# Kernel optimization log

Hardware: AMD Instinct MI355X
Metric: run time of the kernel (lower is better)

## Reference

```python
import jax, jax.numpy as jnp
import numpy as np

T = 5          # temporal_window_size
B = 512        # batch (graphs per timestep)
NA = 16        # num_agents (nodes per graph)
S = 64         # num_belief_states
A = 16         # action_dim
HID = 64       # hidden_dim per head
H = 4          # num_attn_heads
FD = HID * H   # 256, feature_dim
LAT = 128      # latent_dim
N = B * NA     # total nodes per timestep
FIN = S + A    # node feature dim
NEG_SLOPE = 0.2


def _edge_index():
    i, j = np.meshgrid(np.arange(NA), np.arange(NA), indexing='ij')
    m = i != j
    src_l, dst_l = i[m], j[m]                      # 240 intra-clique edges
    off = (np.arange(B) * NA)[:, None]
    src = (src_l[None] + off).ravel()
    dst = (dst_l[None] + off).ravel()
    loops = np.arange(N)                           # PyG GATConv add_self_loops=True
    src = np.concatenate([src, loops])
    dst = np.concatenate([dst, loops])
    return jnp.asarray(np.stack([src, dst]), dtype=jnp.int64)


def setup_inputs() -> dict:
    key = jax.random.key(0)
    ks = jax.random.split(key, 24)
    xav = lambda k, shp: jax.random.normal(k, shp, jnp.float32) * np.float32(np.sqrt(2.0 / (shp[0] + shp[-1])))
    return {
        'signals': jax.random.normal(ks[0], (T, B, S), jnp.float32),
        'neighbor_actions': jax.random.normal(ks[1], (T, B, NA * A), jnp.float32),
        'lin_w0': xav(ks[2], (FD, FIN)),
        'att_src0': xav(ks[3], (H, HID)),
        'att_dst0': xav(ks[4], (H, HID)),
        'bias0': jnp.zeros((FD,), jnp.float32),
        'lin_w1': xav(ks[5], (FD, FD)),
        'att_src1': xav(ks[6], (H, HID)),
        'att_dst1': xav(ks[7], (H, HID)),
        'bias1': jnp.zeros((FD,), jnp.float32),
        'in_proj_w': xav(ks[8], (3 * FD, FD)),
        'in_proj_b': jnp.zeros((3 * FD,), jnp.float32),
        'out_proj_w': xav(ks[9], (FD, FD)),
        'out_proj_b': jnp.zeros((FD,), jnp.float32),
        'w_mean': xav(ks[10], (LAT, FD)),
        'b_mean': jnp.zeros((LAT,), jnp.float32),
        'w_logvar': xav(ks[11], (LAT, FD)),
        'b_logvar': jnp.zeros((LAT,), jnp.float32),
        'w_belief': xav(ks[12], (S, FD)),
        'b_belief': jnp.zeros((S,), jnp.float32),
        'edge_index': _edge_index(),
    }


def _segment_softmax(e, seg, num_segments):
    # e: [E, T, H]; softmax over edges sharing the same target node.
    m = jax.ops.segment_max(e, seg, num_segments=num_segments)
    e = jnp.exp(e - m[seg])
    s = jax.ops.segment_sum(e, seg, num_segments=num_segments)
    return e / s[seg]


def _gat(x, src, dst, w, a_src, a_dst, b):
    # x: [N, T, Fin] -> [N, T, H*HID]   (PyG GATConv, concat heads)
    xl = jnp.einsum('ntf,of->nto', x, w).reshape(N, T, H, HID)
    e_src = jnp.einsum('nthc,hc->nth', xl, a_src)[src]   # [E, T, H]
    e_dst = jnp.einsum('nthc,hc->nth', xl, a_dst)[dst]
    e = jax.nn.leaky_relu(e_src + e_dst, NEG_SLOPE)
    alpha = _segment_softmax(e, dst, N)                  # per-target softmax
    out = jax.ops.segment_sum(alpha[..., None] * xl[src], dst, num_segments=N)
    return out.reshape(N, T, FD) + b


def reference(signals, neighbor_actions, lin_w0, att_src0, att_dst0, bias0,
              lin_w1, att_src1, att_dst1, bias1, in_proj_w, in_proj_b,
              out_proj_w, out_proj_b, w_mean, b_mean, w_logvar, b_logvar,
              w_belief, b_belief, edge_index):
    # --- _construct_graph (vectorized over time window + batch) ---
    acts = neighbor_actions.reshape(T, B, NA, A)
    beliefs = jnp.zeros((T, B, NA, S), signals.dtype).at[:, :, 0, :].set(signals)
    nodes = jnp.concatenate([beliefs, acts], -1).reshape(T, N, FIN)
    nodes = jnp.transpose(nodes, (1, 0, 2))              # [N, T, FIN]
    src, dst = edge_index[0], edge_index[1]
    x = jax.nn.relu(_gat(nodes, src, dst, lin_w0, att_src0, att_dst0, bias0))
    x = jax.nn.relu(_gat(x, src, dst, lin_w1, att_src1, att_dst1, bias1))
    # --- ego-node sequence: nodes 0, NA, 2*NA, ... ---
    seq = x[::NA]                                        # [B, T, FD]
    # --- temporal MultiheadAttention (batch_first, eval) ---
    qkv = seq @ in_proj_w.T + in_proj_b
    q, k, v = jnp.split(qkv, 3, axis=-1)
    dh = FD // H
    q = q.reshape(B, T, H, dh); k = k.reshape(B, T, H, dh); v = v.reshape(B, T, H, dh)
    scores = jnp.einsum('bqhd,bkhd->bhqk', q, k) / jnp.sqrt(jnp.asarray(dh, seq.dtype))
    # torch float attn_mask is ADDITIVE: mask[i,j]=1 if j<=i else 0
    mask = (jnp.arange(T)[:, None] >= jnp.arange(T)[None, :]).astype(seq.dtype)
    attn = jax.nn.softmax(scores + mask[None, None], axis=-1)
    ctx = jnp.einsum('bhqk,bkhd->bqhd', attn, v).reshape(B, T, FD)
    ctx = ctx @ out_proj_w.T + out_proj_b
    feat = ctx[:, -1]                                    # [B, FD]
    # --- heads ---
    mean = feat @ w_mean.T + b_mean
    logvar = feat @ w_logvar.T + b_logvar
    belief = jax.nn.softmax(feat @ w_belief.T + b_belief, axis=-1)
    return (mean, logvar, belief)
```

## Files before the change

### kernel.cpp

```cpp
#include <hip/hip_runtime.h>
#include <hip/hip_bf16.h>


__device__ __forceinline__ float wave_sum64(float v) {
    #pragma unroll
    for (int off = 32; off > 0; off >>= 1) v += __shfl_xor(v, off, 64);
    return v;
}
__device__ __forceinline__ float wave_max64(float v) {
    #pragma unroll
    for (int off = 32; off > 0; off >>= 1) v = fmaxf(v, __shfl_xor(v, off, 64));
    return v;
}

__global__ __launch_bounds__(256) void k_pre(
    const float* __restrict__ w0, const float* __restrict__ w1,
    const float* __restrict__ wip, const float* __restrict__ wop,
    const float* __restrict__ wm, const float* __restrict__ wlv,
    const float* __restrict__ wb,
    const float* __restrict__ as0, const float* __restrict__ ad0,
    const float* __restrict__ as1, const float* __restrict__ ad1,
    float* __restrict__ tws,
    float* __restrict__ u1, float* __restrict__ ud1,
    float* __restrict__ pa0, float* __restrict__ pd0)
{
    const int tid = threadIdx.x;
    if (blockIdx.x < 1680) {
        int i = blockIdx.x * 256 + tid;
        float v;
        if (i < 16384) {
            int k = i >> 8, n = i & 255;
            v = w0[n * 80 + k];
        } else if (i < 20480) {
            int j = i - 16384; int k = j >> 8, n = j & 255;
            v = w0[n * 80 + 64 + k];
        } else if (i < 86016) {
            int j = i - 20480; int k = j >> 8, n = j & 255;
            v = w1[n * 256 + k];
        } else if (i < 282624) {
            int j = i - 86016; int k = j / 768, n = j - k * 768;
            v = wip[n * 256 + k];
        } else if (i < 348160) {
            int j = i - 282624; int k = j >> 8, n = j & 255;
            v = wop[n * 256 + k];
        } else {
            int j = i - 348160; int k = j / 320, o = j - k * 320;
            if (o < 128)      v = wm[o * 256 + k];
            else if (o < 256) v = wlv[(o - 128) * 256 + k];
            else              v = wb[(o - 256) * 256 + k];
        }
        tws[i] = v;
        return;
    }
    for (int q = 0; q < 4; q++) {
        int idx = q * 256 + tid;
        int h = idx >> 8, k = idx & 255;
        float su = 0.f, sd = 0.f;
        for (int c = 0; c < 64; c++) {
            float wv = w1[(h * 64 + c) * 256 + k];
            su = fmaf(as1[h * 64 + c], wv, su);
            sd = fmaf(ad1[h * 64 + c], wv, sd);
        }
        u1[idx] = su; ud1[idx] = sd;
    }
    if (tid < 64) {
        int h = tid >> 4, k = tid & 15;
        float su = 0.f, sd = 0.f;
        for (int c = 0; c < 64; c++) {
            float wv = w0[(h * 64 + c) * 80 + 64 + k];
            su = fmaf(as0[h * 64 + c], wv, su);
            sd = fmaf(ad0[h * 64 + c], wv, sd);
        }
        pa0[tid] = su; pd0[tid] = sd;
    }
}

__global__ __launch_bounds__(256) void k_gat(
    const float* __restrict__ sig,
    const float* __restrict__ nact,
    const float* __restrict__ W0sT,
    const float* __restrict__ W0aT,
    const float* __restrict__ W1T,
    const float* __restrict__ u1g, const float* __restrict__ ud1g,
    const float* __restrict__ pa0g, const float* __restrict__ pd0g,
    const float* __restrict__ as0, const float* __restrict__ ad0,
    const float* __restrict__ b0, const float* __restrict__ b1,
    float* __restrict__ seqf)
{
    __shared__ __align__(16) char smem[37168];
    float* actL    = (float*)(smem + 0);
    float* sigL    = (float*)(smem + 1024);
    float* u1L     = (float*)(smem + 1280);
    float* ud1L    = (float*)(smem + 5440);
    float* pa0L    = (float*)(smem + 9600);
    float* pd0L    = (float*)(smem + 9856);
    float* sSL     = (float*)(smem + 10112);
    float* dSL     = (float*)(smem + 10128);
    float* es0L    = (float*)(smem + 10144);
    float* ed0L    = (float*)(smem + 10400);
    float* espL    = (float*)(smem + 10656);
    float* es1L    = (float*)(smem + 11680);
    float* edpL    = (float*)(smem + 11936);
    float* edL     = (float*)(smem + 12000);
    float* alpha1L = (float*)(smem + 12016);
    float* a0L     = (float*)(smem + 12272);
    float* zL      = (float*)(smem + 16368);
    float* x1L     = (float*)(smem + 20528);

    const int tid = threadIdx.x;
    const int bg = blockIdx.x;
    const int b = bg / 5, g = bg - b * 5;
    const int n = tid, w = tid >> 6, lane = tid & 63;

    if (tid < 64) sigL[tid] = sig[(g * 512 + b) * 64 + tid];
    actL[tid] = nact[(g * 512 + b) * 256 + tid];
    #pragma unroll
    for (int q = 0; q < 4; q++) {
        int idx = q * 256 + tid;
        int h = idx >> 8, k = idx & 255;
        u1L[h * 260 + k] = u1g[idx];
        ud1L[h * 260 + k] = ud1g[idx];
    }
    if (tid >= 64 && tid < 128) {
        pa0L[tid - 64] = pa0g[tid - 64];
        pd0L[tid - 64] = pd0g[tid - 64];
    }
    __syncthreads();

    float S = 0.f;
    {
        const float4* sig4 = (const float4*)sigL;
        #pragma unroll 4
        for (int i = 0; i < 16; i++) {
            float4 sv = sig4[i];
            S = fmaf(sv.x, W0sT[(i * 4 + 0) * 256 + n], S);
            S = fmaf(sv.y, W0sT[(i * 4 + 1) * 256 + n], S);
            S = fmaf(sv.z, W0sT[(i * 4 + 2) * 256 + n], S);
            S = fmaf(sv.w, W0sT[(i * 4 + 3) * 256 + n], S);
        }
        float ps = wave_sum64(S * as0[n]);
        float pd_ = wave_sum64(S * ad0[n]);
        if (lane == 0) { sSL[w] = ps; dSL[w] = pd_; }
    }
    __syncthreads();

    if (tid < 64) {
        int m = tid >> 2, h = tid & 3;
        float su = (m == 0) ? sSL[h] : 0.f;
        float sd = (m == 0) ? dSL[h] : 0.f;
        #pragma unroll
        for (int k = 0; k < 16; k++) {
            float av = actL[m * 16 + k];
            su = fmaf(av, pa0L[h * 16 + k], su);
            sd = fmaf(av, pd0L[h * 16 + k], sd);
        }
        es0L[m * 4 + h] = su; ed0L[m * 4 + h] = sd;
    }
    __syncthreads();

    if (tid < 64) {
        int h = tid >> 4, j = tid & 15;
        float ej = ed0L[j * 4 + h];
        float e[16], m = -1e30f;
        #pragma unroll
        for (int s = 0; s < 16; s++) {
            float x = es0L[s * 4 + h] + ej;
            x = (x >= 0.f) ? x : 0.2f * x;
            e[s] = x; m = fmaxf(m, x);
        }
        float sum = 0.f;
        #pragma unroll
        for (int s = 0; s < 16; s++) { e[s] = __expf(e[s] - m); sum += e[s]; }
        float inv = 1.f / sum;
        float4* a04 = (float4*)(a0L + h * 256 + j * 16);
        #pragma unroll
        for (int s4 = 0; s4 < 4; s4++)
            a04[s4] = make_float4(e[s4 * 4] * inv, e[s4 * 4 + 1] * inv,
                                  e[s4 * 4 + 2] * inv, e[s4 * 4 + 3] * inv);
    }
    __syncthreads();

    float x1r[16];
    {
        const int h = w;
        float wr[16];
        #pragma unroll
        for (int k = 0; k < 16; k++) wr[k] = W0aT[k * 256 + n];
        const float4* act4 = (const float4*)actL;
        float xl0r[16];
        #pragma unroll
        for (int s = 0; s < 16; s++) {
            float a = 0.f;
            #pragma unroll
            for (int q = 0; q < 4; q++) {
                float4 av = act4[s * 4 + q];
                a = fmaf(av.x, wr[q * 4 + 0], a);
                a = fmaf(av.y, wr[q * 4 + 1], a);
                a = fmaf(av.z, wr[q * 4 + 2], a);
                a = fmaf(av.w, wr[q * 4 + 3], a);
            }
            xl0r[s] = a;
        }
        xl0r[0] += S;
        const float b0v = b0[n];
        const float4* a04 = (const float4*)(a0L + h * 256);
        #pragma unroll
        for (int j = 0; j < 16; j++) {
            float acc = b0v;
            #pragma unroll
            for (int s4 = 0; s4 < 4; s4++) {
                float4 a4 = a04[j * 4 + s4];
                acc = fmaf(a4.x, xl0r[s4 * 4 + 0], acc);
                acc = fmaf(a4.y, xl0r[s4 * 4 + 1], acc);
                acc = fmaf(a4.z, xl0r[s4 * 4 + 2], acc);
                acc = fmaf(a4.w, xl0r[s4 * 4 + 3], acc);
            }
            x1r[j] = fmaxf(acc, 0.f);
            x1L[j * 260 + n] = x1r[j];
        }
    }
    __syncthreads();

    {
        const int m = tid & 15, h = (tid >> 4) & 3, p = tid >> 6;
        const float4* x4p = (const float4*)(x1L + m * 260 + p * 64);
        const float4* u4p = (const float4*)(u1L + h * 260 + p * 64);
        float a = 0.f;
        #pragma unroll
        for (int i = 0; i < 16; i++) {
            float4 xv = x4p[i], uv = u4p[i];
            a = fmaf(xv.x, uv.x, a);
            a = fmaf(xv.y, uv.y, a);
            a = fmaf(xv.z, uv.z, a);
            a = fmaf(xv.w, uv.w, a);
        }
        espL[m * 16 + h * 4 + p] = a;
        if (m == 0) {
            const float4* ud4p = (const float4*)(ud1L + h * 260 + p * 64);
            float ad = 0.f;
            #pragma unroll
            for (int i = 0; i < 16; i++) {
                float4 xv = x4p[i], uv = ud4p[i];
                ad = fmaf(xv.x, uv.x, ad);
                ad = fmaf(xv.y, uv.y, ad);
                ad = fmaf(xv.z, uv.z, ad);
                ad = fmaf(xv.w, uv.w, ad);
            }
            edpL[h * 4 + p] = ad;
        }
    }
    __syncthreads();
    if (tid < 64) {
        int m = tid >> 2, h = tid & 3;
        const float* e = espL + m * 16 + h * 4;
        es1L[m * 4 + h] = e[0] + e[1] + e[2] + e[3];
    }
    if (tid < 4)
        edL[tid] = edpL[tid * 4] + edpL[tid * 4 + 1] + edpL[tid * 4 + 2] + edpL[tid * 4 + 3];
    __syncthreads();

    if (tid < 4) {
        int h = tid;
        float ej = edL[h];
        float e[16], m = -1e30f;
        #pragma unroll
        for (int s = 0; s < 16; s++) {
            float x = es1L[s * 4 + h] + ej;
            x = (x >= 0.f) ? x : 0.2f * x;
            e[s] = x; m = fmaxf(m, x);
        }
        float sum = 0.f;
        #pragma unroll
        for (int s = 0; s < 16; s++) { e[s] = __expf(e[s] - m); sum += e[s]; }
        float inv = 1.f / sum;
        #pragma unroll
        for (int s = 0; s < 16; s++) alpha1L[h * 16 + s] = e[s] * inv;
    }
    __syncthreads();

    {
        const float4* a14 = (const float4*)alpha1L;
        #pragma unroll
        for (int hh = 0; hh < 4; hh++) {
            float zv = 0.f;
            #pragma unroll
            for (int s4 = 0; s4 < 4; s4++) {
                float4 a4 = a14[hh * 4 + s4];
                zv = fmaf(a4.x, x1r[s4 * 4 + 0], zv);
                zv = fmaf(a4.y, x1r[s4 * 4 + 1], zv);
                zv = fmaf(a4.z, x1r[s4 * 4 + 2], zv);
                zv = fmaf(a4.w, x1r[s4 * 4 + 3], zv);
            }
            zL[hh * 260 + n] = zv;
        }
    }
    __syncthreads();

    {
        const float4* zh = (const float4*)(zL + w * 260);
        float acc = b1[n];
        #pragma unroll 8
        for (int i = 0; i < 64; i++) {
            float4 z4 = zh[i];
            acc = fmaf(z4.x, W1T[(i * 4 + 0) * 256 + n], acc);
            acc = fmaf(z4.y, W1T[(i * 4 + 1) * 256 + n], acc);
            acc = fmaf(z4.z, W1T[(i * 4 + 2) * 256 + n], acc);
            acc = fmaf(z4.w, W1T[(i * 4 + 3) * 256 + n], acc);
        }
        seqf[bg * 256 + n] = fmaxf(acc, 0.f);
    }
}

__global__ __launch_bounds__(768) void k_stage2(
    const float* __restrict__ seqf,
    const float* __restrict__ wipT,
    const float* __restrict__ bip,
    const float* __restrict__ wopT,
    const float* __restrict__ bop,
    const float* __restrict__ whT,
    const float* __restrict__ bm, const float* __restrict__ blv,
    const float* __restrict__ bb,
    float* __restrict__ out)
{
    __shared__ float sseq[2][5][256];
    __shared__ float kL[2][5][256], vL[2][5][256], qL[2][256];
    __shared__ float ctxL[2][256], featL[2][256];
    __shared__ float beliefL[2][64];
    const int tid = threadIdx.x;
    const int b0 = blockIdx.x * 2;

    {
        float* sflat = &sseq[0][0][0];
        for (int i = tid; i < 2560; i += 768)
            sflat[i] = seqf[b0 * 1280 + i];
    }
    __syncthreads();

    {
        const int kind = tid >> 8, n = tid & 255;
        if (kind == 0) {
            float a0 = 0.f, a1 = 0.f;
            for (int k = 0; k < 256; k++) {
                float wv = wipT[k * 768 + n];
                a0 = fmaf(sseq[0][4][k], wv, a0);
                a1 = fmaf(sseq[1][4][k], wv, a1);
            }
            float bv = bip[n];
            qL[0][n] = a0 + bv; qL[1][n] = a1 + bv;
        } else {
            const float* wcol = wipT + kind * 256 + n;
            float acc[2][5];
            #pragma unroll
            for (int gb = 0; gb < 2; gb++)
                #pragma unroll
                for (int t = 0; t < 5; t++) acc[gb][t] = 0.f;
            for (int k = 0; k < 256; k++) {
                float wv = wcol[k * 768];
                #pragma unroll
                for (int gb = 0; gb < 2; gb++) {
                    #pragma unroll
                    for (int t = 0; t < 5; t++)
                        acc[gb][t] = fmaf(sseq[gb][t][k], wv, acc[gb][t]);
                }
            }
            float bv = bip[kind * 256 + n];
            float* dst = (kind == 1) ? &kL[0][0][0] : &vL[0][0][0];
            #pragma unroll
            for (int gb = 0; gb < 2; gb++)
                #pragma unroll
                for (int t = 0; t < 5; t++)
                    dst[gb * 1280 + t * 256 + n] = acc[gb][t] + bv;
        }
    }
    __syncthreads();

    if (tid < 512) {
        const int gb = tid >> 8, col = tid & 255;
        float q4 = qL[gb][col];
        float sc[5];
        #pragma unroll
        for (int t = 0; t < 5; t++)
            sc[t] = wave_sum64(q4 * kL[gb][t][col]) * 0.125f;
        float m = sc[0];
        #pragma unroll
        for (int t = 1; t < 5; t++) m = fmaxf(m, sc[t]);
        float p[5], sum = 0.f;
        #pragma unroll
        for (int t = 0; t < 5; t++) { p[t] = __expf(sc[t] - m); sum += p[t]; }
        float inv = 1.f / sum, cv = 0.f;
        #pragma unroll
        for (int t = 0; t < 5; t++) cv = fmaf(p[t], vL[gb][t][col], cv);
        ctxL[gb][col] = cv * inv;
    }
    __syncthreads();

    if (tid < 512) {
        const int gb = tid >> 8, n = tid & 255;
        float acc = 0.f;
        for (int k = 0; k < 256; k++)
            acc = fmaf(ctxL[gb][k], wopT[k * 256 + n], acc);
        featL[gb][n] = acc + bop[n];
    }
    __syncthreads();

    if (tid < 640) {
        const int gb = tid / 320, j = tid - gb * 320;
        float acc = 0.f;
        for (int k = 0; k < 256; k++)
            acc = fmaf(featL[gb][k], whT[k * 320 + j], acc);
        if (j < 128) {
            out[(b0 + gb) * 128 + j] = acc + bm[j];
        } else if (j < 256) {
            out[65536 + (b0 + gb) * 128 + (j - 128)] = acc + blv[j - 128];
        } else {
            beliefL[gb][j - 256] = acc + bb[j - 256];
        }
    }
    __syncthreads();

    if (tid < 128) {
        int gb = tid >> 6, lane = tid & 63;
        float lg = beliefL[gb][lane];
        float m = wave_max64(lg);
        float e = __expf(lg - m);
        float s = wave_sum64(e);
        out[131072 + (b0 + gb) * 64 + lane] = e / s;
    }
}

extern "C" void kernel_launch(void* const* d_in, const int* in_sizes, int n_in,
                              void* d_out, int out_size, void* d_ws, size_t ws_size,
                              hipStream_t stream) {
    const float* sig  = (const float*)d_in[0];
    const float* nact = (const float*)d_in[1];
    const float* w0   = (const float*)d_in[2];
    const float* as0  = (const float*)d_in[3];
    const float* ad0  = (const float*)d_in[4];
    const float* b0   = (const float*)d_in[5];
    const float* w1   = (const float*)d_in[6];
    const float* as1  = (const float*)d_in[7];
    const float* ad1  = (const float*)d_in[8];
    const float* b1   = (const float*)d_in[9];
    const float* wip  = (const float*)d_in[10];
    const float* bip  = (const float*)d_in[11];
    const float* wop  = (const float*)d_in[12];
    const float* bop  = (const float*)d_in[13];
    const float* wm   = (const float*)d_in[14];
    const float* bm   = (const float*)d_in[15];
    const float* wlv  = (const float*)d_in[16];
    const float* blv  = (const float*)d_in[17];
    const float* wb   = (const float*)d_in[18];
    const float* bb   = (const float*)d_in[19];

    float* ws    = (float*)d_ws;
    float* seqf  = ws;
    float* tws   = ws + 655360;
    float* W0sT  = tws;
    float* W0aT  = tws + 16384;
    float* W1T   = tws + 20480;
    float* wipT  = tws + 86016;
    float* wopT  = tws + 282624;
    float* whT   = tws + 348160;
    float* u1    = ws + 1085440;
    float* ud1   = ws + 1086464;
    float* pa0   = ws + 1087488;
    float* pd0   = ws + 1087552;

    k_pre   <<<1681, 256, 0, stream>>>(w0, w1, wip, wop, wm, wlv, wb,
                                       as0, ad0, as1, ad1,
                                       tws, u1, ud1, pa0, pd0);
    k_gat   <<<2560, 256, 0, stream>>>(sig, nact, W0sT, W0aT, W1T,
                                       u1, ud1, pa0, pd0, as0, ad0, b0, b1, seqf);
    k_stage2<<<256, 768, 0, stream>>>(seqf, wipT, bip, wopT, bop, whT,
                                      bm, blv, bb, (float*)d_out);
}
```

Before: 201.2 us.

## Make GAT layer-0 attention per-wave and batch weight loads in k_gat

Layer-0 attention logits and softmax are now computed inside each wave for its own head, using the wave-wide reductions directly. This removes three block-wide barriers and the sS/dS staging buffers. The layer-1 softmax is folded into wave 0, which drops one more barrier. Global weight loads for W0s and W1 are grouped 16 at a time to expose more memory-level parallelism, and launch bounds request 4 blocks per CU, which may constrain register allocation.

```diff
diff --git a/kernel.cpp b/kernel.cpp
--- a/kernel.cpp
+++ b/kernel.cpp
@@ -75,7 +75,7 @@
     }
 }
 
-__global__ __launch_bounds__(256) void k_gat(
+__global__ __launch_bounds__(256, 4) void k_gat(
     const float* __restrict__ sig,
     const float* __restrict__ nact,
     const float* __restrict__ W0sT,
@@ -87,25 +87,22 @@
     const float* __restrict__ b0, const float* __restrict__ b1,
     float* __restrict__ seqf)
 {
-    __shared__ __align__(16) char smem[37168];
+    __shared__ __align__(16) char smem[37120];
     float* actL    = (float*)(smem + 0);
     float* sigL    = (float*)(smem + 1024);
     float* u1L     = (float*)(smem + 1280);
     float* ud1L    = (float*)(smem + 5440);
     float* pa0L    = (float*)(smem + 9600);
     float* pd0L    = (float*)(smem + 9856);
-    float* sSL     = (float*)(smem + 10112);
-    float* dSL     = (float*)(smem + 10128);
-    float* es0L    = (float*)(smem + 10144);
-    float* ed0L    = (float*)(smem + 10400);
-    float* espL    = (float*)(smem + 10656);
-    float* es1L    = (float*)(smem + 11680);
-    float* edpL    = (float*)(smem + 11936);
-    float* edL     = (float*)(smem + 12000);
-    float* alpha1L = (float*)(smem + 12016);
-    float* a0L     = (float*)(smem + 12272);
-    float* zL      = (float*)(smem + 16368);
-    float* x1L     = (float*)(smem + 20528);
+    float* es0w    = (float*)(smem + 10112);
+    float* ed0w    = (float*)(smem + 10368);
+    float* espL    = (float*)(smem + 10624);
+    float* es1L    = (float*)(smem + 11648);
+    float* edpL    = (float*)(smem + 11904);
+    float* alpha1L = (float*)(smem + 11968);
+    float* a0L     = (float*)(smem + 12224);
+    float* zL      = (float*)(smem + 16320);
+    float* x1L     = (float*)(smem + 20480);
 
     const int tid = threadIdx.x;
     const int bg = blockIdx.x;
@@ -130,59 +127,70 @@
     float S = 0.f;
     {
         const float4* sig4 = (const float4*)sigL;
-        #pragma unroll 4
-        for (int i = 0; i < 16; i++) {
-            float4 sv = sig4[i];
-            S = fmaf(sv.x, W0sT[(i * 4 + 0) * 256 + n], S);
-            S = fmaf(sv.y, W0sT[(i * 4 + 1) * 256 + n], S);
-            S = fmaf(sv.z, W0sT[(i * 4 + 2) * 256 + n], S);
-            S = fmaf(sv.w, W0sT[(i * 4 + 3) * 256 + n], S);
-        }
-        float ps = wave_sum64(S * as0[n]);
-        float pd_ = wave_sum64(S * ad0[n]);
-        if (lane == 0) { sSL[w] = ps; dSL[w] = pd_; }
-    }
-    __syncthreads();
-
-    if (tid < 64) {
-        int m = tid >> 2, h = tid & 3;
-        float su = (m == 0) ? sSL[h] : 0.f;
-        float sd = (m == 0) ? dSL[h] : 0.f;
-        #pragma unroll
-        for (int k = 0; k < 16; k++) {
-            float av = actL[m * 16 + k];
-            su = fmaf(av, pa0L[h * 16 + k], su);
-            sd = fmaf(av, pd0L[h * 16 + k], sd);
-        }
-        es0L[m * 4 + h] = su; ed0L[m * 4 + h] = sd;
-    }
-    __syncthreads();
-
-    if (tid < 64) {
-        int h = tid >> 4, j = tid & 15;
-        float ej = ed0L[j * 4 + h];
+        #pragma unroll
+        for (int i = 0; i < 4; i++) {
+            float wv[16];
+            #pragma unroll
+            for (int j = 0; j < 16; j++)
+                wv[j] = W0sT[(i * 16 + j) * 256 + n];
+            #pragma unroll
+            for (int q = 0; q < 4; q++) {
+                float4 sv = sig4[i * 4 + q];
+                S = fmaf(wv[q * 4 + 0], sv.x, S);
+                S = fmaf(wv[q * 4 + 1], sv.y, S);
+                S = fmaf(wv[q * 4 + 2], sv.z, S);
+                S = fmaf(wv[q * 4 + 3], sv.w, S);
+            }
+        }
+    }
+    const float sS = wave_sum64(S * as0[n]);
+    const float dS = wave_sum64(S * ad0[n]);
+
+    if (lane < 16) {
+        const int m = lane;
+        float su = (m == 0) ? sS : 0.f;
+        float sd = (m == 0) ? dS : 0.f;
+        const float4* act4 = (const float4*)(actL + m * 16);
+        const float4* pa4  = (const float4*)(pa0L + w * 16);
+        const float4* pd4  = (const float4*)(pd0L + w * 16);
+        #pragma unroll
+        for (int q = 0; q < 4; q++) {
+            float4 av = act4[q], pv = pa4[q], dv = pd4[q];
+            su = fmaf(av.x, pv.x, su); su = fmaf(av.y, pv.y, su);
+            su = fmaf(av.z, pv.z, su); su = fmaf(av.w, pv.w, su);
+            sd = fmaf(av.x, dv.x, sd); sd = fmaf(av.y, dv.y, sd);
+            sd = fmaf(av.z, dv.z, sd); sd = fmaf(av.w, dv.w, sd);
+        }
+        es0w[w * 16 + m] = su;
+        ed0w[w * 16 + m] = sd;
+    }
+    if (lane < 16) {
+        const int j = lane;
+        float ej = ed0w[w * 16 + j];
         float e[16], m = -1e30f;
-        #pragma unroll
-        for (int s = 0; s < 16; s++) {
-            float x = es0L[s * 4 + h] + ej;
-            x = (x >= 0.f) ? x : 0.2f * x;
-            e[s] = x; m = fmaxf(m, x);
+        const float4* es4 = (const float4*)(es0w + w * 16);
+        #pragma unroll
+        for (int s4 = 0; s4 < 4; s4++) {
+            float4 ev = es4[s4];
+            float x;
+            x = ev.x + ej; x = (x >= 0.f) ? x : 0.2f * x; e[s4*4+0] = x; m = fmaxf(m, x);
+            x = ev.y + ej; x = (x >= 0.f) ? x : 0.2f * x; e[s4*4+1] = x; m = fmaxf(m, x);
+            x = ev.z + ej; x = (x >= 0.f) ? x : 0.2f * x; e[s4*4+2] = x; m = fmaxf(m, x);
+            x = ev.w + ej; x = (x >= 0.f) ? x : 0.2f * x; e[s4*4+3] = x; m = fmaxf(m, x);
         }
         float sum = 0.f;
         #pragma unroll
         for (int s = 0; s < 16; s++) { e[s] = __expf(e[s] - m); sum += e[s]; }
         float inv = 1.f / sum;
-        float4* a04 = (float4*)(a0L + h * 256 + j * 16);
+        float4* a04 = (float4*)(a0L + w * 256 + j * 16);
         #pragma unroll
         for (int s4 = 0; s4 < 4; s4++)
             a04[s4] = make_float4(e[s4 * 4] * inv, e[s4 * 4 + 1] * inv,
                                   e[s4 * 4 + 2] * inv, e[s4 * 4 + 3] * inv);
     }
-    __syncthreads();
 
     float x1r[16];
     {
-        const int h = w;
         float wr[16];
         #pragma unroll
         for (int k = 0; k < 16; k++) wr[k] = W0aT[k * 256 + n];
@@ -203,7 +211,7 @@
         }
         xl0r[0] += S;
         const float b0v = b0[n];
-        const float4* a04 = (const float4*)(a0L + h * 256);
+        const float4* a04 = (const float4*)(a0L + w * 256);
         #pragma unroll
         for (int j = 0; j < 16; j++) {
             float acc = b0v;
@@ -250,31 +258,30 @@
         }
     }
     __syncthreads();
-    if (tid < 64) {
-        int m = tid >> 2, h = tid & 3;
-        const float* e = espL + m * 16 + h * 4;
-        es1L[m * 4 + h] = e[0] + e[1] + e[2] + e[3];
-    }
-    if (tid < 4)
-        edL[tid] = edpL[tid * 4] + edpL[tid * 4 + 1] + edpL[tid * 4 + 2] + edpL[tid * 4 + 3];
-    __syncthreads();
-
-    if (tid < 4) {
-        int h = tid;
-        float ej = edL[h];
-        float e[16], m = -1e30f;
-        #pragma unroll
-        for (int s = 0; s < 16; s++) {
-            float x = es1L[s * 4 + h] + ej;
-            x = (x >= 0.f) ? x : 0.2f * x;
-            e[s] = x; m = fmaxf(m, x);
-        }
-        float sum = 0.f;
-        #pragma unroll
-        for (int s = 0; s < 16; s++) { e[s] = __expf(e[s] - m); sum += e[s]; }
-        float inv = 1.f / sum;
-        #pragma unroll
-        for (int s = 0; s < 16; s++) alpha1L[h * 16 + s] = e[s] * inv;
+
+    if (w == 0) {
+        {
+            const int m = lane >> 2, h = lane & 3;
+            const float* e = espL + m * 16 + h * 4;
+            es1L[m * 4 + h] = e[0] + e[1] + e[2] + e[3];
+        }
+        if (lane < 4) {
+            const int h = lane;
+            float ej = edpL[h * 4] + edpL[h * 4 + 1] + edpL[h * 4 + 2] + edpL[h * 4 + 3];
+            float e[16], m = -1e30f;
+            #pragma unroll
+            for (int s = 0; s < 16; s++) {
+                float x = es1L[s * 4 + h] + ej;
+                x = (x >= 0.f) ? x : 0.2f * x;
+                e[s] = x; m = fmaxf(m, x);
+            }
+            float sum = 0.f;
+            #pragma unroll
+            for (int s = 0; s < 16; s++) { e[s] = __expf(e[s] - m); sum += e[s]; }
+            float inv = 1.f / sum;
+            #pragma unroll
+            for (int s = 0; s < 16; s++) alpha1L[h * 16 + s] = e[s] * inv;
+        }
     }
     __syncthreads();
 
@@ -299,13 +306,19 @@
     {
         const float4* zh = (const float4*)(zL + w * 260);
         float acc = b1[n];
-        #pragma unroll 8
-        for (int i = 0; i < 64; i++) {
-            float4 z4 = zh[i];
-            acc = fmaf(z4.x, W1T[(i * 4 + 0) * 256 + n], acc);
-            acc = fmaf(z4.y, W1T[(i * 4 + 1) * 256 + n], acc);
-            acc = fmaf(z4.z, W1T[(i * 4 + 2) * 256 + n], acc);
-            acc = fmaf(z4.w, W1T[(i * 4 + 3) * 256 + n], acc);
+        for (int i = 0; i < 16; i++) {
+            float wv[16];
+            #pragma unroll
+            for (int j = 0; j < 16; j++)
+                wv[j] = W1T[(i * 16 + j) * 256 + n];
+            #pragma unroll
+            for (int q = 0; q < 4; q++) {
+                float4 z4 = zh[i * 4 + q];
+                acc = fmaf(wv[q * 4 + 0], z4.x, acc);
+                acc = fmaf(wv[q * 4 + 1], z4.y, acc);
+                acc = fmaf(wv[q * 4 + 2], z4.z, acc);
+                acc = fmaf(wv[q * 4 + 3], z4.w, acc);
+            }
         }
         seqf[bg * 256 + n] = fmaxf(acc, 0.f);
     }
```

Result: no change. 199.8 us (-0.7%).
